# Optimization experiments

Measured on AMD Instinct MI355X. Metric: run time of the kernel, lower is better.

## Reference

```python
import jax, jax.numpy as jnp
import numpy as np

N = 100000      # nodes
E = 800000      # edges
P = 200000      # number of subgraph permutations
L = 16          # lrp_length
D = 64          # lrp_out_dim (== lrp_in_dim)
PL = P * L
LEN_SEQ = 4     # int(sqrt(L))
NUM_BOND = 4


def setup_inputs() -> dict:
    key = jax.random.key(0)
    ks = jax.random.split(key, 16)
    inp = {}
    inp["nfeat"] = jax.random.normal(ks[0], (N, D), jnp.float32)
    inp["degs"] = jax.random.uniform(ks[1], (N,), jnp.float32) * 8.0 + 1.0
    inp["n2p_val"] = jnp.ones((PL,), jnp.float32)
    inp["e2p_val"] = jnp.ones((PL,), jnp.float32)
    inp["pool_val"] = jax.random.uniform(ks[2], (P,), jnp.float32)
    inp["weights"] = jax.random.normal(ks[3], (D, D, L), jnp.float32)
    inp["bias"] = jnp.zeros((1, D), jnp.float32)
    inp["w_deg0"] = jax.random.normal(ks[4], (2 * D, LEN_SEQ), jnp.float32) * 0.3
    inp["b_deg0"] = jnp.zeros((2 * D,), jnp.float32)
    inp["w_deg1"] = jax.random.normal(ks[5], (D, 2 * D), jnp.float32) * 0.1
    inp["b_deg1"] = jnp.zeros((D,), jnp.float32)
    inp["w_lin"] = jax.random.normal(ks[6], (D, D), jnp.float32) * 0.1
    inp["b_lin"] = jnp.zeros((D,), jnp.float32)
    inp["bond_emb"] = jax.random.normal(ks[7], (NUM_BOND, D), jnp.float32)
    inp["edge_feat_idx"] = jax.random.randint(ks[8], (E,), 0, NUM_BOND, jnp.int32)
    inp["n2p_row"] = jnp.arange(PL, dtype=jnp.int32)
    inp["n2p_col"] = jax.random.randint(ks[9], (PL,), 0, N, jnp.int32)
    inp["e2p_row"] = jnp.arange(PL, dtype=jnp.int32)
    inp["e2p_col"] = jax.random.randint(ks[10], (PL,), 0, E, jnp.int32)
    inp["pool_row"] = jax.random.randint(ks[11], (P,), 0, N, jnp.int32)
    inp["pool_col"] = jnp.arange(P, dtype=jnp.int32)
    return inp


def _spmm(row, col, val, x, m):
    # COO spmm: out[r] = sum_{nnz with row==r} val * x[col]
    return jax.ops.segment_sum(val[:, None] * x[col], row, num_segments=m)


def reference(nfeat, degs, n2p_val, e2p_val, pool_val, weights, bias,
              w_deg0, b_deg0, w_deg1, b_deg1, w_lin, b_lin, bond_emb,
              edge_feat_idx, n2p_row, n2p_col, e2p_row, e2p_col,
              pool_row, pool_col):
    n = nfeat.shape[0]
    pl = n2p_row.shape[0]
    d = weights.shape[0]
    l = weights.shape[2]
    p = pl // l
    len_seq = int(round(l ** 0.5))

    efeat = bond_emb[edge_feat_idx]                                  # [E, D]
    perm = _spmm(n2p_row, n2p_col, n2p_val, nfeat, pl) \
         + _spmm(e2p_row, e2p_col, e2p_val, efeat, pl)               # [P*L, D]
    deg_perm = _spmm(n2p_row, n2p_col, n2p_val, degs[:, None], pl)   # [P*L, 1]

    x = perm.reshape(p, l, d)                                        # [P, L, D]
    deg_sel = deg_perm.reshape(p, l)[:, ::len_seq + 1]               # [P, len_seq]

    h = jnp.einsum('pab,bca->pc', x, weights) + bias                 # [P, D]
    h = jax.nn.relu(h) @ w_lin.T + b_lin                             # linear(relu(.))

    g = jax.nn.relu(deg_sel @ w_deg0.T + b_deg0) @ w_deg1.T + b_deg1  # [P, D]
    h = h * g

    out = _spmm(pool_row, pool_col, pool_val, h, n)                  # [N, D]
    return out
```

## Files before the change

### kernel.cpp

```cpp
#include <hip/hip_runtime.h>
#include <hip/hip_bf16.h>

typedef __attribute__((ext_vector_type(8))) __bf16 bf16x8;
typedef __attribute__((ext_vector_type(4))) float floatx4;
typedef __attribute__((ext_vector_type(4))) int intx4;
typedef __attribute__((ext_vector_type(4))) unsigned uintx4;

constexpr int N_NODES = 100000;
constexpr int P_PERM  = 200000;

constexpr size_t W2F_OFF  = 0;
constexpr size_t WLF_OFF  = 131072;
constexpr size_t WD1F_OFF = 139264;
constexpr size_t BE_OFF   = 155648;
constexpr size_t NFBF_OFF = 3355648;
constexpr size_t WS_NEED_FULL = 3355648 + (size_t)N_NODES * 64 * 2;

__global__ void prep_all_kernel(float4* __restrict__ out,
                                const float* __restrict__ weights,
                                const float* __restrict__ w_lin,
                                const float* __restrict__ w_deg1,
                                const float* __restrict__ nfeat,
                                const int* __restrict__ e2p_col,
                                const int* __restrict__ edge_feat_idx,
                                __bf16* __restrict__ ws_bf) {
  int b = blockIdx.x;
  int t = threadIdx.x;
  if (b < 6250) {
    out[b * 256 + t] = make_float4(0.f, 0.f, 0.f, 0.f);
  } else if (b < 6554) {
    int i = (b - 6250) * 256 + t;
    if (i < 65536) {
      int j = i & 7, l = (i >> 3) & 63, ct = (i >> 9) & 3, ks = (i >> 11) & 1, a = i >> 12;
      int k = ks * 32 + (l >> 4) * 8 + j;
      int c = ct * 16 + (l & 15);
      ws_bf[W2F_OFF / 2 + i] = (__bf16)weights[k * 1024 + c * 16 + a];
    } else if (i < 65536 + 4096) {
      int i2 = i - 65536;
      int j = i2 & 7, l = (i2 >> 3) & 63, ct = (i2 >> 9) & 3, ks = (i2 >> 11) & 1;
      int k = ks * 32 + (l >> 4) * 8 + j;
      int c = ct * 16 + (l & 15);
      ws_bf[WLF_OFF / 2 + i2] = (__bf16)w_lin[c * 64 + k];
    } else if (i < 65536 + 4096 + 8192) {
      int i3 = i - 65536 - 4096;
      int j = i3 & 7, l = (i3 >> 3) & 63, ct = (i3 >> 9) & 3, ks = (i3 >> 11) & 3;
      int k = ks * 32 + (l >> 4) * 8 + j;
      int c = ct * 16 + (l & 15);
      ws_bf[WD1F_OFF / 2 + i3] = (__bf16)w_deg1[c * 128 + k];
    }
  } else if (b < 9679) {
    int i = (b - 6554) * 256 + t;
    if (i < N_NODES * 8) {
      float4 a = *(const float4*)(nfeat + (size_t)i * 8);
      float4 c = *(const float4*)(nfeat + (size_t)i * 8 + 4);
      bf16x8 o;
      o[0] = (__bf16)a.x; o[1] = (__bf16)a.y; o[2] = (__bf16)a.z; o[3] = (__bf16)a.w;
      o[4] = (__bf16)c.x; o[5] = (__bf16)c.y; o[6] = (__bf16)c.z; o[7] = (__bf16)c.w;
      *(bf16x8*)(ws_bf + NFBF_OFF / 2 + (size_t)i * 8) = o;
    }
  } else {
    int i = (b - 9679) * 256 + t;
    if (i < P_PERM * 4) {
      int4 ec = ((const int4*)e2p_col)[i];
      unsigned v = (unsigned)(edge_feat_idx[ec.x] & 0xff)
                 | ((unsigned)(edge_feat_idx[ec.y] & 0xff) << 8)
                 | ((unsigned)(edge_feat_idx[ec.z] & 0xff) << 16)
                 | ((unsigned)(edge_feat_idx[ec.w] & 0xff) << 24);
      ((unsigned*)((char*)ws_bf + BE_OFF))[i] = v;
    }
  }
}

template <bool BF16FEAT>
__global__ __launch_bounds__(256, 4) void lrp_mfma_kernel(
    const float* __restrict__ nfeat,
    const float* __restrict__ degs,
    const float* __restrict__ n2p_val,
    const float* __restrict__ e2p_val,
    const float* __restrict__ pool_val,
    const float* __restrict__ bias,
    const float* __restrict__ w_deg0,
    const float* __restrict__ b_deg0,
    const float* __restrict__ b_deg1,
    const float* __restrict__ b_lin,
    const float* __restrict__ bond_emb,
    const int* __restrict__ n2p_col,
    const int* __restrict__ pool_row,
    const __bf16* __restrict__ ws_bf,
    float* __restrict__ out) {
  __shared__ __align__(16) char fraglds[2][8192];
  __shared__ __align__(16) __bf16 sbond[4][72];
  __shared__ __align__(16) float swdeg0[128][4];
  __shared__ float sbd0[128];
  __shared__ float sbias[64];
  __shared__ float sblin[64];
  __shared__ float sbd1[64];
  __shared__ __align__(16) __bf16 hs[4][2][16][72];

  const int t = threadIdx.x;
  const int w = t >> 6;
  const int l = t & 63;
  const int m = l & 15;
  const int q = l >> 4;
  const int pb0 = blockIdx.x * 256 + w * 32;
  const int pbase = blockIdx.x * 128 + w * 32;
  int pb[2]  = {pbase, pbase + 16};
  bool valid[2];
  int pbc[2];
  #pragma unroll
  for (int pt = 0; pt < 2; ++pt) {
    valid[pt] = pb[pt] < P_PERM;
    pbc[pt] = valid[pt] ? pb[pt] : (P_PERM - 16);
  }

  if (t < 256) sbond[t >> 6][t & 63] = (__bf16)bond_emb[t];
  if (t < 128) {
    *(float4*)&swdeg0[t][0] = *(const float4*)(w_deg0 + t * 4);
    sbd0[t] = b_deg0[t];
  } else if (t < 192) {
    int c = t - 128;
    sbias[c] = bias[c]; sblin[c] = b_lin[c]; sbd1[c] = b_deg1[c];
  }

  const __bf16* __restrict__ nfbf = ws_bf + NFBF_OFF / 2;
  const bf16x8* __restrict__ WLv  = (const bf16x8*)(ws_bf + WLF_OFF / 2);
  const bf16x8* __restrict__ WD1v = (const bf16x8*)(ws_bf + WD1F_OFF / 2);
  const unsigned* __restrict__ bep = (const unsigned*)((const char*)ws_bf + BE_OFF);
  const char* __restrict__ W2bytes = (const char*)ws_bf + W2F_OFF;

  intx4 nvx[2], evx[2], ncx[2];
  int bex[2];
  #pragma unroll
  for (int pt = 0; pt < 2; ++pt) {
    size_t rb = (size_t)pbc[pt] * 16;
    nvx[pt] = *(const intx4*)(n2p_val + rb + 4 * l);
    evx[pt] = *(const intx4*)(e2p_val + rb + 4 * l);
    ncx[pt] = *(const intx4*)(n2p_col + rb + 4 * l);
    bex[pt] = (int)bep[(size_t)pbc[pt] * 4 + l];
  }
  const int selbase = m * 16;

  auto stage = [&](int a, int buf) {
    #pragma unroll
    for (int j = 0; j < 2; ++j) {
      const char* g = W2bytes + (size_t)a * 8192 + (w * 2 + j) * 1024 + l * 16;
      char* lds = &fraglds[buf][(w * 2 + j) * 1024];
      __builtin_amdgcn_global_load_lds(
          (const __attribute__((address_space(1))) unsigned*)g,
          (__attribute__((address_space(3))) unsigned*)lds, 16, 0, 0);
    }
  };
  auto gath = [&](int nc, bf16x8* g) {
    #pragma unroll
    for (int ks = 0; ks < 2; ++ks) {
      int k0 = ks * 32 + q * 8;
      if (BF16FEAT) {
        g[ks] = *(const bf16x8*)(nfbf + (size_t)nc * 64 + k0);
      } else {
        float4 n0 = *(const float4*)(nfeat + (size_t)nc * 64 + k0);
        float4 n1 = *(const float4*)(nfeat + (size_t)nc * 64 + k0 + 4);
        bf16x8 o;
        o[0] = (__bf16)n0.x; o[1] = (__bf16)n0.y; o[2] = (__bf16)n0.z; o[3] = (__bf16)n0.w;
        o[4] = (__bf16)n1.x; o[5] = (__bf16)n1.y; o[6] = (__bf16)n1.z; o[7] = (__bf16)n1.w;
        g[ks] = o;
      }
    }
  };

  floatx4 acc[2][4] = {};
  float dsreg[2][4];
  float nv0[2], ev0[2];
  int nc0[2], be0[2];
  bf16x8 g_cur[2][2], g_nxt[2][2];

  #pragma unroll
  for (int pt = 0; pt < 2; ++pt) {
    nv0[pt] = __int_as_float(__builtin_amdgcn_ds_bpermute(selbase, nvx[pt][0]));
    ev0[pt] = __int_as_float(__builtin_amdgcn_ds_bpermute(selbase, evx[pt][0]));
    nc0[pt] = __builtin_amdgcn_ds_bpermute(selbase, ncx[pt][0]);
    be0[pt] = (__builtin_amdgcn_ds_bpermute(selbase, bex[pt])) & 0xff;
    gath(nc0[pt], g_cur[pt]);
  }
  stage(0, 0);
  __syncthreads();

  #pragma unroll
  for (int a = 0; a < 16; ++a) {
    const int buf = a & 1;
    float nv1[2], ev1[2];
    int nc1[2], be1[2];
    if (a < 15) {
      const int an = a + 1;
      const int sel1 = selbase + (an >> 2) * 4;
      const int sl = an & 3;
      #pragma unroll
      for (int pt = 0; pt < 2; ++pt) {
        nv1[pt] = __int_as_float(__builtin_amdgcn_ds_bpermute(sel1, nvx[pt][sl]));
        ev1[pt] = __int_as_float(__builtin_amdgcn_ds_bpermute(sel1, evx[pt][sl]));
        nc1[pt] = __builtin_amdgcn_ds_bpermute(sel1, ncx[pt][sl]);
        be1[pt] = (__builtin_amdgcn_ds_bpermute(sel1, bex[pt]) >> (sl * 8)) & 0xff;
      }
      stage(a + 1, buf ^ 1);
      #pragma unroll
      for (int pt = 0; pt < 2; ++pt) gath(nc1[pt], g_nxt[pt]);
    }

    bf16x8 afv[2][2];
    #pragma unroll
    for (int pt = 0; pt < 2; ++pt) {
      #pragma unroll
      for (int ks = 0; ks < 2; ++ks) {
        bf16x8 eb = *(const bf16x8*)&sbond[be0[pt]][ks * 32 + q * 8];
        bf16x8 af;
        #pragma unroll
        for (int j = 0; j < 8; ++j)
          af[j] = (__bf16)fmaf(nv0[pt], (float)g_cur[pt][ks][j],
                               ev0[pt] * (float)eb[j]);
        afv[pt][ks] = af;
      }
    }
    #pragma unroll
    for (int ks = 0; ks < 2; ++ks)
      #pragma unroll
      for (int ct = 0; ct < 4; ++ct) {
        bf16x8 frag = *(const bf16x8*)&fraglds[buf][((ks * 4 + ct) * 64 + l) * 16];
        acc[0][ct] = __builtin_amdgcn_mfma_f32_16x16x32_bf16(afv[0][ks], frag, acc[0][ct], 0, 0, 0);
        acc[1][ct] = __builtin_amdgcn_mfma_f32_16x16x32_bf16(afv[1][ks], frag, acc[1][ct], 0, 0, 0);
      }

    if (a == 0 || a == 5 || a == 10 || a == 15) {
      const int jj = a / 5;
      #pragma unroll
      for (int pt = 0; pt < 2; ++pt)
        dsreg[pt][jj] = nv0[pt] * degs[nc0[pt]];
    }

    if (a < 15) {
      __syncthreads();
      #pragma unroll
      for (int pt = 0; pt < 2; ++pt) {
        nv0[pt] = nv1[pt]; ev0[pt] = ev1[pt]; nc0[pt] = nc1[pt]; be0[pt] = be1[pt];
        g_cur[pt][0] = g_nxt[pt][0]; g_cur[pt][1] = g_nxt[pt][1];
      }
    }
  }

  floatx4 acc2[2][4] = {};
  {
    #pragma unroll
    for (int pt = 0; pt < 2; ++pt)
      #pragma unroll
      for (int ct = 0; ct < 4; ++ct) {
        float bv = sbias[ct * 16 + m];
        #pragma unroll
        for (int rr = 0; rr < 4; ++rr)
          hs[w][pt][q * 4 + rr][ct * 16 + m] =
              (__bf16)fmaxf(acc[pt][ct][rr] + bv, 0.0f);
      }
    #pragma unroll
    for (int pt = 0; pt < 2; ++pt)
      #pragma unroll
      for (int ks = 0; ks < 2; ++ks) {
        bf16x8 af2 = *(const bf16x8*)&hs[w][pt][m][ks * 32 + q * 8];
        #pragma unroll
        for (int ct = 0; ct < 4; ++ct) {
          bf16x8 frag = WLv[(ks * 4 + ct) * 64 + l];
          acc2[pt][ct] = __builtin_amdgcn_mfma_f32_16x16x32_bf16(af2, frag, acc2[pt][ct], 0, 0, 0);
        }
      }
  }

  floatx4 gacc[2][4] = {};
  #pragma unroll
  for (int ks = 0; ks < 4; ++ks) {
    const int k0 = ks * 32 + q * 8;
    bf16x8 af[2];
    #pragma unroll
    for (int j = 0; j < 8; ++j) {
      int k = k0 + j;
      float4 wr = *(const float4*)&swdeg0[k][0];
      float bk = sbd0[k];
      #pragma unroll
      for (int pt = 0; pt < 2; ++pt) {
        float v = bk;
        v = fmaf(dsreg[pt][0], wr.x, v);
        v = fmaf(dsreg[pt][1], wr.y, v);
        v = fmaf(dsreg[pt][2], wr.z, v);
        v = fmaf(dsreg[pt][3], wr.w, v);
        af[pt][j] = (__bf16)fmaxf(v, 0.0f);
      }
    }
    #pragma unroll
    for (int ct = 0; ct < 4; ++ct) {
      bf16x8 frag = WD1v[(ks * 4 + ct) * 64 + l];
      gacc[0][ct] = __builtin_amdgcn_mfma_f32_16x16x32_bf16(af[0], frag, gacc[0][ct], 0, 0, 0);
      gacc[1][ct] = __builtin_amdgcn_mfma_f32_16x16x32_bf16(af[1], frag, gacc[1][ct], 0, 0, 0);
    }
  }

  #pragma unroll
  for (int pt = 0; pt < 2; ++pt) {
    if (!valid[pt]) continue;
    intx4   pr4 = *(const intx4*)(pool_row + pb[pt] + q * 4);
    floatx4 pv4 = *(const floatx4*)(pool_val + pb[pt] + q * 4);
    #pragma unroll
    for (int rr = 0; rr < 4; ++rr) {
      float* orow = out + (size_t)pr4[rr] * 64;
      float pv = pv4[rr];
      #pragma unroll
      for (int ct = 0; ct < 4; ++ct) {
        float h2 = (acc2[pt][ct][rr] + sblin[ct * 16 + m]) *
                   (gacc[pt][ct][rr] + sbd1[ct * 16 + m]);
        atomicAdd(orow + ct * 16 + m, pv * h2);
      }
    }
  }
}

extern "C" void kernel_launch(void* const* d_in, const int* in_sizes, int n_in,
                              void* d_out, int out_size, void* d_ws, size_t ws_size,
                              hipStream_t stream) {
  const float* nfeat    = (const float*)d_in[0];
  const float* degs     = (const float*)d_in[1];
  const float* n2p_val  = (const float*)d_in[2];
  const float* e2p_val  = (const float*)d_in[3];
  const float* pool_val = (const float*)d_in[4];
  const float* weights  = (const float*)d_in[5];
  const float* bias     = (const float*)d_in[6];
  const float* w_deg0   = (const float*)d_in[7];
  const float* b_deg0   = (const float*)d_in[8];
  const float* w_deg1   = (const float*)d_in[9];
  const float* b_deg1   = (const float*)d_in[10];
  const float* w_lin    = (const float*)d_in[11];
  const float* b_lin    = (const float*)d_in[12];
  const float* bond_emb = (const float*)d_in[13];
  const int* edge_feat_idx = (const int*)d_in[14];
  const int* n2p_col    = (const int*)d_in[16];
  const int* e2p_col    = (const int*)d_in[18];
  const int* pool_row   = (const int*)d_in[19];

  float* out = (float*)d_out;
  __bf16* ws_bf = (__bf16*)d_ws;

  prep_all_kernel<<<12804, 256, 0, stream>>>((float4*)out, weights, w_lin,
                                             w_deg1, nfeat, e2p_col,
                                             edge_feat_idx, ws_bf);

  int grid = (P_PERM + 127) / 128;
  if (ws_size >= WS_NEED_FULL) {
    lrp_mfma_kernel<true><<<grid, 256, 0, stream>>>(
        nfeat, degs, n2p_val, e2p_val, pool_val, bias, w_deg0, b_deg0,
        b_deg1, b_lin, bond_emb, n2p_col, pool_row, ws_bf, out);
  } else {
    lrp_mfma_kernel<false><<<grid, 256, 0, stream>>>(
        nfeat, degs, n2p_val, e2p_val, pool_val, bias, w_deg0, b_deg0,
        b_deg1, b_lin, bond_emb, n2p_col, pool_row, ws_bf, out);
  }
}
```

Measured before the change: 307.5 us.

## Replace atomic pooling scatter with CSR build and gather-based pool kernel

Instead of each MFMA block atomically adding pooled h values into the output, the kernel now writes per-permutation h2 rows to a workspace buffer. A histogram, three-stage scan and scatter build a CSR index of pool_row. A separate pool kernel then gathers and sums rows per node without atomics, and writes zeros for empty nodes, so the output zeroing is skipped. This removes 12.8M float atomics but adds five small kernels, an extra 51MB write and read of h2, and atomics for the histogram and scatter. It only takes effect when the workspace is large enough.

```diff
diff --git a/kernel.cpp b/kernel.cpp
--- a/kernel.cpp
+++ b/kernel.cpp
@@ -4,7 +4,6 @@
 typedef __attribute__((ext_vector_type(8))) __bf16 bf16x8;
 typedef __attribute__((ext_vector_type(4))) float floatx4;
 typedef __attribute__((ext_vector_type(4))) int intx4;
-typedef __attribute__((ext_vector_type(4))) unsigned uintx4;
 
 constexpr int N_NODES = 100000;
 constexpr int P_PERM  = 200000;
@@ -14,7 +13,16 @@
 constexpr size_t WD1F_OFF = 139264;
 constexpr size_t BE_OFF   = 155648;
 constexpr size_t NFBF_OFF = 3355648;
-constexpr size_t WS_NEED_FULL = 3355648 + (size_t)N_NODES * 64 * 2;
+constexpr size_t H2_OFF   = 16155648;
+constexpr size_t RP_OFF   = 67355648;
+constexpr size_t CUR_OFF  = 67755664;
+constexpr size_t CIDX_OFF = 68155664;
+constexpr size_t CSUM_OFF = 68955664;
+constexpr size_t WS_NEED_BF16 = 16155648;
+constexpr size_t WS_NEED_CSR  = 68956000;
+
+constexpr int SCAN_CHUNK = 2048;
+constexpr int NCHUNK = 49;
 
 __global__ void prep_all_kernel(float4* __restrict__ out,
                                 const float* __restrict__ weights,
@@ -23,11 +31,12 @@
                                 const float* __restrict__ nfeat,
                                 const int* __restrict__ e2p_col,
                                 const int* __restrict__ edge_feat_idx,
-                                __bf16* __restrict__ ws_bf) {
+                                __bf16* __restrict__ ws_bf,
+                                int do_zero_out) {
   int b = blockIdx.x;
   int t = threadIdx.x;
   if (b < 6250) {
-    out[b * 256 + t] = make_float4(0.f, 0.f, 0.f, 0.f);
+    if (do_zero_out) out[b * 256 + t] = make_float4(0.f, 0.f, 0.f, 0.f);
   } else if (b < 6554) {
     int i = (b - 6250) * 256 + t;
     if (i < 65536) {
@@ -58,7 +67,7 @@
       o[4] = (__bf16)c.x; o[5] = (__bf16)c.y; o[6] = (__bf16)c.z; o[7] = (__bf16)c.w;
       *(bf16x8*)(ws_bf + NFBF_OFF / 2 + (size_t)i * 8) = o;
     }
-  } else {
+  } else if (b < 12804) {
     int i = (b - 9679) * 256 + t;
     if (i < P_PERM * 4) {
       int4 ec = ((const int4*)e2p_col)[i];
@@ -68,10 +77,118 @@
                  | ((unsigned)(edge_feat_idx[ec.w] & 0xff) << 24);
       ((unsigned*)((char*)ws_bf + BE_OFF))[i] = v;
     }
-  }
-}
-
-template <bool BF16FEAT>
+  } else {
+    int i = (b - 12804) * 256 + t;
+    if (i < N_NODES) ((int*)((char*)ws_bf + CUR_OFF))[i] = 0;
+  }
+}
+
+__global__ void hist_kernel(const int* __restrict__ pool_row, int* __restrict__ hist) {
+  int i = blockIdx.x * 256 + threadIdx.x;
+  if (i < P_PERM) atomicAdd(&hist[pool_row[i]], 1);
+}
+
+__global__ void scan1_kernel(const int* __restrict__ hist, int* __restrict__ csum) {
+  __shared__ int red[256];
+  int b = blockIdx.x, t = threadIdx.x;
+  int s = 0;
+  #pragma unroll
+  for (int j = 0; j < 8; ++j) {
+    int i = b * SCAN_CHUNK + t * 8 + j;
+    s += (i < N_NODES) ? hist[i] : 0;
+  }
+  red[t] = s;
+  __syncthreads();
+  for (int off = 128; off > 0; off >>= 1) {
+    if (t < off) red[t] += red[t + off];
+    __syncthreads();
+  }
+  if (t == 0) csum[b] = red[0];
+}
+
+__global__ void scan2_kernel(int* __restrict__ csum, int* __restrict__ row_ptr) {
+  if (threadIdx.x == 0) {
+    int acc = 0;
+    for (int i = 0; i < NCHUNK; ++i) {
+      int v = csum[i];
+      csum[i] = acc;
+      acc += v;
+    }
+    row_ptr[N_NODES] = acc;
+  }
+}
+
+__global__ void scan3_kernel(const int* __restrict__ csum,
+                             int* __restrict__ hist_cursor,
+                             int* __restrict__ row_ptr) {
+  __shared__ int sc[257];
+  int b = blockIdx.x, t = threadIdx.x;
+  int v[8];
+  int s = 0;
+  #pragma unroll
+  for (int j = 0; j < 8; ++j) {
+    int i = b * SCAN_CHUNK + t * 8 + j;
+    v[j] = (i < N_NODES) ? hist_cursor[i] : 0;
+    s += v[j];
+  }
+  sc[t + 1] = s;
+  if (t == 0) sc[0] = 0;
+  __syncthreads();
+  for (int off = 1; off < 256; off <<= 1) {
+    int x = (t >= off) ? sc[t + 1 - off] : 0;
+    __syncthreads();
+    sc[t + 1] += x;
+    __syncthreads();
+  }
+  int excl = csum[b] + sc[t];
+  #pragma unroll
+  for (int j = 0; j < 8; ++j) {
+    int i = b * SCAN_CHUNK + t * 8 + j;
+    if (i < N_NODES) {
+      row_ptr[i] = excl;
+      hist_cursor[i] = excl;
+    }
+    excl += v[j];
+  }
+}
+
+__global__ void scatter_kernel(const int* __restrict__ pool_row,
+                               int* __restrict__ cursor,
+                               int* __restrict__ cidx) {
+  int i = blockIdx.x * 256 + threadIdx.x;
+  if (i < P_PERM) {
+    int pos = atomicAdd(&cursor[pool_row[i]], 1);
+    cidx[pos] = i;
+  }
+}
+
+__global__ __launch_bounds__(256, 8) void pool_kernel(
+    const int* __restrict__ row_ptr, const int* __restrict__ cidx,
+    const float* __restrict__ pool_val, const float* __restrict__ h2,
+    float* __restrict__ out) {
+  int g = blockIdx.x * 256 + threadIdx.x;
+  int n = g >> 2, qd = g & 3;
+  if (n >= N_NODES) return;
+  int s = row_ptr[n], e = row_ptr[n + 1];
+  floatx4 a0 = {0,0,0,0}, a1 = {0,0,0,0}, a2 = {0,0,0,0}, a3 = {0,0,0,0};
+  for (int i = s; i < e; ++i) {
+    int p = cidx[i];
+    float pv = pool_val[p];
+    const float* hr = h2 + (size_t)p * 64 + qd * 16;
+    floatx4 h0 = *(const floatx4*)(hr + 0);
+    floatx4 h1 = *(const floatx4*)(hr + 4);
+    floatx4 h2v = *(const floatx4*)(hr + 8);
+    floatx4 h3 = *(const floatx4*)(hr + 12);
+    a0 += pv * h0; a1 += pv * h1; a2 += pv * h2v; a3 += pv * h3;
+  }
+  float* orow = out + (size_t)n * 64 + qd * 16;
+  *(floatx4*)(orow + 0) = a0;
+  *(floatx4*)(orow + 4) = a1;
+  *(floatx4*)(orow + 8) = a2;
+  *(floatx4*)(orow + 12) = a3;
+}
+
+template <bool BF16FEAT, bool CSR>
 __global__ __launch_bounds__(256, 4) void lrp_mfma_kernel(
     const float* __restrict__ nfeat,
     const float* __restrict__ degs,
@@ -87,6 +204,7 @@
     const int* __restrict__ n2p_col,
     const int* __restrict__ pool_row,
     const __bf16* __restrict__ ws_bf,
+    float* __restrict__ h2out,
     float* __restrict__ out) {
   __shared__ __align__(16) char fraglds[2][8192];
   __shared__ __align__(16) __bf16 sbond[4][72];
@@ -102,9 +220,8 @@
   const int l = t & 63;
   const int m = l & 15;
   const int q = l >> 4;
-  const int pb0 = blockIdx.x * 256 + w * 32;
   const int pbase = blockIdx.x * 128 + w * 32;
-  int pb[2]  = {pbase, pbase + 16};
+  int pb[2] = {pbase, pbase + 16};
   bool valid[2];
   int pbc[2];
   #pragma unroll
@@ -298,20 +415,37 @@
     }
   }
 
-  #pragma unroll
-  for (int pt = 0; pt < 2; ++pt) {
-    if (!valid[pt]) continue;
-    intx4   pr4 = *(const intx4*)(pool_row + pb[pt] + q * 4);
-    floatx4 pv4 = *(const floatx4*)(pool_val + pb[pt] + q * 4);
-    #pragma unroll
-    for (int rr = 0; rr < 4; ++rr) {
-      float* orow = out + (size_t)pr4[rr] * 64;
-      float pv = pv4[rr];
-      #pragma unroll
-      for (int ct = 0; ct < 4; ++ct) {
-        float h2 = (acc2[pt][ct][rr] + sblin[ct * 16 + m]) *
-                   (gacc[pt][ct][rr] + sbd1[ct * 16 + m]);
-        atomicAdd(orow + ct * 16 + m, pv * h2);
+  if (CSR) {
+    #pragma unroll
+    for (int pt = 0; pt < 2; ++pt) {
+      if (!valid[pt]) continue;
+      #pragma unroll
+      for (int rr = 0; rr < 4; ++rr) {
+        float* hrow = h2out + (size_t)(pb[pt] + q * 4 + rr) * 64 + m;
+        #pragma unroll
+        for (int ct = 0; ct < 4; ++ct) {
+          float h2 = (acc2[pt][ct][rr] + sblin[ct * 16 + m]) *
+                     (gacc[pt][ct][rr] + sbd1[ct * 16 + m]);
+          hrow[ct * 16] = h2;
+        }
+      }
+    }
+  } else {
+    #pragma unroll
+    for (int pt = 0; pt < 2; ++pt) {
+      if (!valid[pt]) continue;
+      intx4   pr4 = *(const intx4*)(pool_row + pb[pt] + q * 4);
+      floatx4 pv4 = *(const floatx4*)(pool_val + pb[pt] + q * 4);
+      #pragma unroll
+      for (int rr = 0; rr < 4; ++rr) {
+        float* orow = out + (size_t)pr4[rr] * 64;
+        float pv = pv4[rr];
+        #pragma unroll
+        for (int ct = 0; ct < 4; ++ct) {
+          float h2 = (acc2[pt][ct][rr] + sblin[ct * 16 + m]) *
+                     (gacc[pt][ct][rr] + sbd1[ct * 16 + m]);
+          atomicAdd(orow + ct * 16 + m, pv * h2);
+        }
       }
     }
   }
@@ -341,19 +475,49 @@
 
   float* out = (float*)d_out;
   __bf16* ws_bf = (__bf16*)d_ws;
-
-  prep_all_kernel<<<12804, 256, 0, stream>>>((float4*)out, weights, w_lin,
+  char* wsb = (char*)d_ws;
+
+  bool bf16feat = ws_size >= WS_NEED_BF16;
+  bool csr = ws_size >= WS_NEED_CSR;
+
+  prep_all_kernel<<<13195, 256, 0, stream>>>((float4*)out, weights, w_lin,
                                              w_deg1, nfeat, e2p_col,
-                                             edge_feat_idx, ws_bf);
+                                             edge_feat_idx, ws_bf, csr ? 0 : 1);
+
+  float* h2buf   = (float*)(wsb + H2_OFF);
+  int* row_ptr   = (int*)(wsb + RP_OFF);
+  int* cursor    = (int*)(wsb + CUR_OFF);
+  int* cidx      = (int*)(wsb + CIDX_OFF);
+  int* csum      = (int*)(wsb + CSUM_OFF);
+
+  if (csr) {
+    hist_kernel<<<(P_PERM + 255) / 256, 256, 0, stream>>>(pool_row, cursor);
+    scan1_kernel<<<NCHUNK, 256, 0, stream>>>(cursor, csum);
+    scan2_kernel<<<1, 64, 0, stream>>>(csum, row_ptr);
+    scan3_kernel<<<NCHUNK, 256, 0, stream>>>(csum, cursor, row_ptr);
+    scatter_kernel<<<(P_PERM + 255) / 256, 256, 0, stream>>>(pool_row, cursor, cidx);
+  }
 
   int grid = (P_PERM + 127) / 128;
-  if (ws_size >= WS_NEED_FULL) {
-    lrp_mfma_kernel<true><<<grid, 256, 0, stream>>>(
-        nfeat, degs, n2p_val, e2p_val, pool_val, bias, w_deg0, b_deg0,
-        b_deg1, b_lin, bond_emb, n2p_col, pool_row, ws_bf, out);
+  if (csr) {
+    if (bf16feat)
+      lrp_mfma_kernel<true, true><<<grid, 256, 0, stream>>>(
+          nfeat, degs, n2p_val, e2p_val, pool_val, bias, w_deg0, b_deg0,
+          b_deg1, b_lin, bond_emb, n2p_col, pool_row, ws_bf, h2buf, out);
+    else
+      lrp_mfma_kernel<false, true><<<grid, 256, 0, stream>>>(
+          nfeat, degs, n2p_val, e2p_val, pool_val, bias, w_deg0, b_deg0,
+          b_deg1, b_lin, bond_emb, n2p_col, pool_row, ws_bf, h2buf, out);
+    pool_kernel<<<(N_NODES * 4 + 255) / 256, 256, 0, stream>>>(
+        row_ptr, cidx, pool_val, h2buf, out);
   } else {
-    lrp_mfma_kernel<false><<<grid, 256, 0, stream>>>(
-        nfeat, degs, n2p_val, e2p_val, pool_val, bias, w_deg0, b_deg0,
-        b_deg1, b_lin, bond_emb, n2p_col, pool_row, ws_bf, out);
-  }
-}
+    if (bf16feat)
+      lrp_mfma_kernel<true, false><<<grid, 256, 0, stream>>>(
+          nfeat, degs, n2p_val, e2p_val, pool_val, bias, w_deg0, b_deg0,
+          b_deg1, b_lin, bond_emb, n2p_col, pool_row, ws_bf, h2buf, out);
+    else
+      lrp_mfma_kernel<false, false><<<grid, 256, 0, stream>>>(
+          nfeat, degs, n2p_val, e2p_val, pool_val, bias, w_deg0, b_deg0,
+          b_deg1, b_lin, bond_emb, n2p_col, pool_row, ws_bf, h2buf, out);
+  }
+}
```

New measurement: 332.2 us. 1.08x slower.
